# Kernel tuning notes

Measured on AMD Instinct MI355X. Metric: run time of the kernel, lower is better.

Reference implementation:

```python
import jax, jax.numpy as jnp
import numpy as np

B, N_LINES, C_FEAT = 16, 200, 64
H_IMG = W_IMG = 256
NUM_BINS = 32
LINE_LENGTH = 64
LINE_LENGTH_MINUS_1_HALF = (LINE_LENGTH - 1) / 2.0
MIN_CONTINUOUS_DISTANCE = 6.0
FUNCTION_AMPLITUDE = 0.43
FUNCTION_SLOPE = 0.5
EPS = 1e-05


def _unnorm(coord, size):
    # torch grid_sample align_corners=False: pixel = ((g + 1) * size - 1) / 2
    return ((coord + 1.0) * size - 1.0) * 0.5


def _gather2d(img, yi, xi, valid):
    # img (B,C,H,W); yi/xi (B,N,L) int32 in-range; zeros padding via valid mask
    g = jax.vmap(lambda im, yy, xx: im[:, yy, xx])(img, yi, xi)  # (B,C,N,L)
    return g * valid[:, None].astype(img.dtype)


def grid_sample_nearest(img, grid):
    _, _, H, W = img.shape
    x = _unnorm(grid[..., 0], W)
    y = _unnorm(grid[..., 1], H)
    xi = jnp.round(x).astype(jnp.int32)
    yi = jnp.round(y).astype(jnp.int32)
    valid = (xi >= 0) & (xi < W) & (yi >= 0) & (yi < H)
    return _gather2d(img, jnp.clip(yi, 0, H - 1), jnp.clip(xi, 0, W - 1), valid)


def grid_sample_bilinear(img, grid):
    _, _, H, W = img.shape
    x = _unnorm(grid[..., 0], W)
    y = _unnorm(grid[..., 1], H)
    x0 = jnp.floor(x)
    y0 = jnp.floor(y)
    wx1 = x - x0
    wy1 = y - y0
    x0i = x0.astype(jnp.int32)
    y0i = y0.astype(jnp.int32)
    out = jnp.zeros(img.shape[:2] + grid.shape[1:3], dtype=img.dtype)
    for dx, wx in ((0, 1.0 - wx1), (1, wx1)):
        for dy, wy in ((0, 1.0 - wy1), (1, wy1)):
            xi = x0i + dx
            yi = y0i + dy
            valid = (xi >= 0) & (xi < W) & (yi >= 0) & (yi < H)
            g = _gather2d(img, jnp.clip(yi, 0, H - 1), jnp.clip(xi, 0, W - 1), valid)
            out = out + g * (wx * wy)[:, None]
    return out


def setup_inputs() -> dict:
    key = jax.random.key(0)
    k = jax.random.split(key, 6)
    image = jax.random.uniform(k[0], (B, 3, H_IMG, W_IMG), dtype=jnp.float32)
    feature = jax.random.normal(k[1], (B, C_FEAT, H_IMG, W_IMG), dtype=jnp.float32)
    pose = jnp.concatenate([
        jnp.tile(jnp.eye(3, dtype=jnp.float32).reshape(1, 9), (B, 1)),
        jnp.tile(jnp.array([[0.0, 0.0, 0.5]], dtype=jnp.float32), (B, 1)),
    ], axis=-1)  # identity rotation, 0.5m in front of camera
    camera_data = jnp.tile(
        jnp.array([[float(W_IMG), float(H_IMG), 300.0, 300.0, 128.0, 128.0]], dtype=jnp.float32),
        (B, 1))  # [w, h, fx, fy, cx, cy]
    centers = jax.random.normal(k[2], (B, N_LINES, 3), dtype=jnp.float32) * 0.05
    normals = jax.random.normal(k[3], (B, N_LINES, 3), dtype=jnp.float32)
    normals = normals / jnp.linalg.norm(normals, axis=-1, keepdims=True)
    dists = jnp.full((B, N_LINES, 2), 0.02, dtype=jnp.float32)
    template_view = jnp.concatenate([centers, normals, dists], axis=-1)  # (B,N,8)
    fore_hist = jax.random.uniform(k[4], (B, NUM_BINS ** 3), dtype=jnp.float32)
    back_hist = jax.random.uniform(k[5], (B, NUM_BINS ** 3), dtype=jnp.float32)
    return {"image": image, "feature": feature,
            "init_body2view_pose_data": pose, "camera_data": camera_data,
            "template_view": template_view, "fore_hist": fore_hist,
            "back_hist": back_hist}


def reference(image, feature, init_body2view_pose_data, camera_data, template_view,
              fore_hist, back_hist):
    R = init_body2view_pose_data[:, :9].reshape(-1, 3, 3)
    t = init_body2view_pose_data[:, 9:]
    centers_in_body = template_view[..., :3]
    normals_in_body = template_view[..., 3:6]
    fg_dist = template_view[..., 6]
    bg_dist = template_view[..., 7]

    # transform / rotate (p3d @ R^T + t)
    centers_in_view = jnp.einsum('bnj,bij->bni', centers_in_body, R) + t[:, None]
    normals_in_view = jnp.einsum('bnj,bij->bni', normals_in_body, R)

    # project_p3d
    z = centers_in_view[..., 2]
    valid1 = z > 1e-4
    p2d = centers_in_view[..., :2] / jnp.maximum(z, 1e-4)[..., None]
    f = camera_data[:, 2:4]
    c = camera_data[:, 4:6]
    size = camera_data[:, :2]
    centers_in_image = p2d * f[:, None] + c[:, None]
    in_b = (centers_in_image >= 0) & (centers_in_image <= size[:, None] - 1)
    centers_valid = valid1 & in_b[..., 0] & in_b[..., 1]

    n2 = normals_in_view[..., :2]
    normals_in_image = n2 / jnp.maximum(jnp.linalg.norm(n2, axis=-1, keepdims=True), 1e-12)

    cur_fg = fg_dist * f[:, 0:1] / z
    cur_bg = bg_dist * f[:, 0:1] / z
    continuous_distance = jnp.minimum(cur_fg, cur_bg)  # fscale = 1 in forward
    valid_data_line = (continuous_distance >= MIN_CONTINUOUS_DISTANCE) & centers_valid

    width, height = feature.shape[2], feature.shape[3]

    # build search-line sample points: (B,N,L,2)
    step = jnp.arange(LINE_LENGTH, dtype=centers_in_image.dtype) - LINE_LENGTH_MINUS_1_HALF
    points = centers_in_image[:, :, None, :] + step[None, None, :, None] * normals_in_image[:, :, None, :]

    def _in_bounds(p):
        return (p[..., 0] >= 0) & (p[..., 0] < width) & (p[..., 1] >= 0) & (p[..., 1] < height)

    valid_data_line = valid_data_line & _in_bounds(points[:, :, 0]) & _in_bounds(points[:, :, -1])

    grid = jnp.stack([points[..., 0] / width * 2 - 1,
                      points[..., 1] / height * 2 - 1], axis=-1)

    # nearest sample of RGB image -> histogram fg/bg probability lookup
    lines_image = grid_sample_nearest(image, grid)  # (B,3,N,L)
    bins = jnp.clip((lines_image * NUM_BINS).astype(jnp.int32), 0, NUM_BINS - 1)
    hist_idx = (bins[:, 0] * NUM_BINS + bins[:, 1]) * NUM_BINS + bins[:, 2]  # (B,N,L)
    pf = jax.vmap(lambda h, i: h[i])(fore_hist, hist_idx)
    pb = jax.vmap(lambda h, i: h[i])(back_hist, hist_idx)
    zero_idx = (pf < EPS) & (pb < EPS)
    pf = jnp.where(zero_idx, EPS, pf)
    pb = jnp.where(zero_idx, EPS, pb)
    psum = pf + pb
    pf = pf / psum  # lines_image_pf_segments (second eps/normalize pass is a no-op)
    pb = pb / psum  # lines_image_pb_segments

    lines_feature = grid_sample_bilinear(feature, grid)  # (B,C,N,L)
    lines_amplitude = jnp.full(pf.shape[:2], FUNCTION_AMPLITUDE, dtype=feature.dtype)
    lines_slope = jnp.full(pf.shape[:2], FUNCTION_SLOPE, dtype=feature.dtype)

    return (normals_in_image, centers_in_image, centers_in_body, pf, pb,
            valid_data_line, lines_amplitude, lines_slope, lines_feature)
```

## Files before the change

### kernel.cpp

```cpp
#include <hip/hip_runtime.h>

#define BN     16
#define NLINES 200
#define CFEAT  64
#define HIMG   256
#define WIMG   256
#define LLEN   64
#define NBINS  32

#define O_NORM   0
#define O_CIMG   6400
#define O_CBODY  12800
#define O_PF     22400
#define O_PB     227200
#define O_VALID  432000
#define O_AMP    435200
#define O_SLOPE  438400
#define O_FEAT   441600

#define NPTS (BN*NLINES*LLEN)

struct LineGeom {
  float cix, ciy;
  float nix, niy;
  float cb0, cb1, cb2;
  bool  vdl;
};

__device__ __forceinline__ LineGeom compute_line(
    const float* __restrict__ pose, const float* __restrict__ cam,
    const float* __restrict__ tv, int b, int n)
{
  const float* P = pose + b*12;
  float R00=P[0],R01=P[1],R02=P[2];
  float R10=P[3],R11=P[4],R12=P[5];
  float R20=P[6],R21=P[7],R22=P[8];
  float t0=P[9], t1=P[10], t2=P[11];
  const float* C = cam + b*6;
  float sx=C[0], sy=C[1], fx=C[2], fy=C[3];
  float cx=C[4], cy=C[5];
  const float* T = tv + (b*NLINES + n)*8;
  float cb0=T[0], cb1=T[1], cb2=T[2];
  float nb0=T[3], nb1=T[4], nb2=T[5];
  float fg=T[6],  bg=T[7];

  float cv0 = R00*cb0 + R01*cb1 + R02*cb2 + t0;
  float cv1 = R10*cb0 + R11*cb1 + R12*cb2 + t1;
  float cv2 = R20*cb0 + R21*cb1 + R22*cb2 + t2;
  float nv0 = R00*nb0 + R01*nb1 + R02*nb2;
  float nv1 = R10*nb0 + R11*nb1 + R12*nb2;

  float z  = cv2;
  float zc = fmaxf(z, 1e-4f);
  float cix = (cv0/zc)*fx + cx;
  float ciy = (cv1/zc)*fy + cy;
  bool inb = (cix >= 0.f) && (cix <= sx - 1.f) && (ciy >= 0.f) && (ciy <= sy - 1.f);
  bool centers_valid = (z > 1e-4f) && inb;

  float nrm = fmaxf(sqrtf(nv0*nv0 + nv1*nv1), 1e-12f);
  float nix = nv0/nrm, niy = nv1/nrm;

  float contd = fminf(fg*fx/z, bg*fx/z);
  bool vdl = (contd >= 6.0f) && centers_valid;

  float px0 = cix + (-31.5f)*nix, py0 = ciy + (-31.5f)*niy;
  float px1 = cix + ( 31.5f)*nix, py1 = ciy + ( 31.5f)*niy;
  vdl = vdl && (px0 >= 0.f) && (px0 < 256.f) && (py0 >= 0.f) && (py0 < 256.f)
            && (px1 >= 0.f) && (px1 < 256.f) && (py1 >= 0.f) && (py1 < 256.f);

  LineGeom g;
  g.cix = cix; g.ciy = ciy; g.nix = nix; g.niy = niy;
  g.cb0 = cb0; g.cb1 = cb1; g.cb2 = cb2; g.vdl = vdl;
  return g;
}

__device__ __forceinline__ void point_xy(const LineGeom& g, int i, float& x, float& y)
{
  float s  = (float)i - 31.5f;
  float px = g.cix + s*g.nix;
  float py = g.ciy + s*g.niy;
  float gx = px/256.0f*2.0f - 1.0f;
  float gy = py/256.0f*2.0f - 1.0f;
  x = ((gx + 1.0f)*256.0f - 1.0f)*0.5f;
  y = ((gy + 1.0f)*256.0f - 1.0f)*0.5f;
}

template <bool PRE>
__device__ __forceinline__ void points_body(const float* __restrict__ image,
                                            const float* __restrict__ pose,
                                            const float* __restrict__ cam,
                                            const float* __restrict__ tv,
                                            const float* __restrict__ fore,
                                            const float* __restrict__ back,
                                            float* __restrict__ out,
                                            int4*  __restrict__ offs,
                                            float4* __restrict__ wts)
{
  int tid = blockIdx.x*256 + threadIdx.x;
  int i  = tid & 63;
  int ln = tid >> 6;
  int n  = ln % NLINES;
  int b  = ln / NLINES;

  LineGeom g = compute_line(pose, cam, tv, b, n);

  float x, y;
  point_xy(g, i, x, y);

  float xr = rintf(x), yr = rintf(y);
  int xi = (int)xr, yi = (int)yr;
  bool v = (xi >= 0) && (xi < WIMG) && (yi >= 0) && (yi < HIMG);
  int xc = min(max(xi, 0), WIMG-1), yc = min(max(yi, 0), HIMG-1);
  const float* ib = image + (size_t)b*3*HIMG*WIMG + yc*WIMG + xc;
  float r0 = v ? ib[0]           : 0.f;
  float r1 = v ? ib[HIMG*WIMG]   : 0.f;
  float r2 = v ? ib[2*HIMG*WIMG] : 0.f;

  int b0 = min(max((int)(r0*32.f), 0), NBINS-1);
  int b1 = min(max((int)(r1*32.f), 0), NBINS-1);
  int b2 = min(max((int)(r2*32.f), 0), NBINS-1);
  int hidx = (b0*NBINS + b1)*NBINS + b2;

  float pf = fore[b*NBINS*NBINS*NBINS + hidx];
  float pb = back[b*NBINS*NBINS*NBINS + hidx];
  if (pf < 1e-5f && pb < 1e-5f) { pf = 1e-5f; pb = 1e-5f; }
  float ps = pf + pb;
  pf /= ps; pb /= ps;

  out[O_PF + ln*LLEN + i] = pf;
  out[O_PB + ln*LLEN + i] = pb;

  if (i == 0) {
    out[O_NORM  + ln*2 + 0] = g.nix;
    out[O_NORM  + ln*2 + 1] = g.niy;
    out[O_CIMG  + ln*2 + 0] = g.cix;
    out[O_CIMG  + ln*2 + 1] = g.ciy;
    out[O_CBODY + ln*3 + 0] = g.cb0;
    out[O_CBODY + ln*3 + 1] = g.cb1;
    out[O_CBODY + ln*3 + 2] = g.cb2;
    out[O_VALID + ln] = g.vdl ? 1.0f : 0.0f;
    out[O_AMP   + ln] = 0.43f;
    out[O_SLOPE + ln] = 0.5f;
  }

  if (PRE) {
    float x0f = floorf(x), y0f = floorf(y);
    float wx1 = x - x0f, wy1 = y - y0f;
    float wx0 = 1.0f - wx1, wy0 = 1.0f - wy1;
    int x0 = (int)x0f, y0 = (int)y0f;
    int x1 = x0 + 1,  y1 = y0 + 1;
    bool vx0 = (x0 >= 0) && (x0 < WIMG);
    bool vx1 = (x1 >= 0) && (x1 < WIMG);
    bool vy0 = (y0 >= 0) && (y0 < HIMG);
    bool vy1 = (y1 >= 0) && (y1 < HIMG);
    float4 w;
    w.x = wx0*wy0 * ((vx0 && vy0) ? 1.f : 0.f);
    w.y = wx1*wy0 * ((vx1 && vy0) ? 1.f : 0.f);
    w.z = wx0*wy1 * ((vx0 && vy1) ? 1.f : 0.f);
    w.w = wx1*wy1 * ((vx1 && vy1) ? 1.f : 0.f);
    int xc0 = min(max(x0,0), WIMG-1), xc1 = min(max(x1,0), WIMG-1);
    int yc0 = min(max(y0,0), HIMG-1), yc1 = min(max(y1,0), HIMG-1);
    int4 o;
    o.x = yc0*WIMG + xc0;
    o.y = yc0*WIMG + xc1;
    o.z = yc1*WIMG + xc0;
    o.w = yc1*WIMG + xc1;
    offs[tid] = o;
    wts[tid]  = w;
  }
}

__global__ __launch_bounds__(256)
void contour_points_pre_kernel(const float* __restrict__ image,
                               const float* __restrict__ pose,
                               const float* __restrict__ cam,
                               const float* __restrict__ tv,
                               const float* __restrict__ fore,
                               const float* __restrict__ back,
                               float* __restrict__ out,
                               int4*  __restrict__ offs,
                               float4* __restrict__ wts)
{
  points_body<true>(image, pose, cam, tv, fore, back, out, offs, wts);
}

__global__ __launch_bounds__(256)
void contour_points_kernel(const float* __restrict__ image,
                           const float* __restrict__ pose,
                           const float* __restrict__ cam,
                           const float* __restrict__ tv,
                           const float* __restrict__ fore,
                           const float* __restrict__ back,
                           float* __restrict__ out)
{
  points_body<false>(image, pose, cam, tv, fore, back, out, nullptr, nullptr);
}

__global__ __launch_bounds__(256)
void contour_gather2_kernel(const float* __restrict__ feature,
                            const int4*  __restrict__ offs,
                            const float4* __restrict__ wts,
                            float* __restrict__ out)
{
  int bid = blockIdx.x;
  int xcd = bid & 7;
  int q   = bid >> 3;
  int j   = q % 50;
  int ug  = q / 50;
  int u   = ug*8 + xcd;
  int b   = u >> 5;
  int c2  = u & 31;
  int c   = c2 << 1;

  int idx = j*256 + (int)threadIdx.x;
  int n   = idx >> 6;
  int i   = idx & 63;

  int p = (b*NLINES + n)*LLEN + i;
  int4   o = offs[p];
  float4 w = wts[p];

  const float* f0 = feature + ((size_t)(b*CFEAT + c) << 16);
  const float* f1 = f0 + (1 << 16);

  float a00 = f0[o.x], a01 = f0[o.y], a02 = f0[o.z], a03 = f0[o.w];
  float a10 = f1[o.x], a11 = f1[o.y], a12 = f1[o.z], a13 = f1[o.w];
  float v0 = w.x*a00 + w.y*a01 + w.z*a02 + w.w*a03;
  float v1 = w.x*a10 + w.y*a11 + w.z*a12 + w.w*a13;

  size_t ob = (size_t)O_FEAT + (((size_t)(b*CFEAT + c))*NLINES + n)*LLEN + i;
  out[ob] = v0;
  out[ob + (size_t)(NLINES*LLEN)] = v1;
}

__global__ __launch_bounds__(256)
void contour_feature_kernel(const float* __restrict__ feature,
                            const float* __restrict__ pose,
                            const float* __restrict__ cam,
                            const float* __restrict__ tv,
                            float* __restrict__ out)
{
  int ln = blockIdx.x;
  int n  = ln % NLINES;
  int b  = ln / NLINES;
  int t  = threadIdx.x;
  int i  = t & 63;
  int w  = t >> 6;

  LineGeom g = compute_line(pose, cam, tv, b, n);
  float x, y;
  point_xy(g, i, x, y);

  float x0f = floorf(x), y0f = floorf(y);
  float wx1 = x - x0f, wy1 = y - y0f;
  float wx0 = 1.0f - wx1, wy0 = 1.0f - wy1;
  int x0 = (int)x0f, y0 = (int)y0f;
  int x1 = x0 + 1,  y1 = y0 + 1;
  bool vx0 = (x0 >= 0) && (x0 < WIMG);
  bool vx1 = (x1 >= 0) && (x1 < WIMG);
  bool vy0 = (y0 >= 0) && (y0 < HIMG);
  bool vy1 = (y1 >= 0) && (y1 < HIMG);
  float w00 = wx0*wy0 * ((vx0 && vy0) ? 1.f : 0.f);
  float w10 = wx1*wy0 * ((vx1 && vy0) ? 1.f : 0.f);
  float w01 = wx0*wy1 * ((vx0 && vy1) ? 1.f : 0.f);
  float w11 = wx1*wy1 * ((vx1 && vy1) ? 1.f : 0.f);
  int xc0 = min(max(x0,0), WIMG-1), xc1 = min(max(x1,0), WIMG-1);
  int yc0 = min(max(y0,0), HIMG-1), yc1 = min(max(y1,0), HIMG-1);
  int off00 = yc0*WIMG + xc0;
  int off10 = yc0*WIMG + xc1;
  int off01 = yc1*WIMG + xc0;
  int off11 = yc1*WIMG + xc1;

  const float* fbase = feature + (size_t)b*CFEAT*HIMG*WIMG;
  size_t obase = (size_t)O_FEAT + (((size_t)b*CFEAT)*NLINES + n)*LLEN + i;

  #pragma unroll
  for (int k = 0; k < 16; ++k) {
    int c = w*16 + k;
    const float* fc = fbase + (size_t)c*HIMG*WIMG;
    float val = w00*fc[off00] + w10*fc[off10]
              + w01*fc[off01] + w11*fc[off11];
    out[obase + (size_t)c*NLINES*LLEN] = val;
  }
}

extern "C" void kernel_launch(void* const* d_in, const int* in_sizes, int n_in,
                              void* d_out, int out_size, void* d_ws, size_t ws_size,
                              hipStream_t stream) {
  const float* image   = (const float*)d_in[0];
  const float* feature = (const float*)d_in[1];
  const float* pose    = (const float*)d_in[2];
  const float* cam     = (const float*)d_in[3];
  const float* tv      = (const float*)d_in[4];
  const float* fore    = (const float*)d_in[5];
  const float* back    = (const float*)d_in[6];
  float* out = (float*)d_out;

  const size_t need = (size_t)NPTS * (sizeof(int4) + sizeof(float4));
  if (ws_size >= need) {
    int4*   offs = (int4*)d_ws;
    float4* wts  = (float4*)((char*)d_ws + (size_t)NPTS*sizeof(int4));
    contour_points_pre_kernel<<<NPTS/256, 256, 0, stream>>>(
        image, pose, cam, tv, fore, back, out, offs, wts);
    contour_gather2_kernel<<<(BN*CFEAT*NLINES*LLEN)/(2*256), 256, 0, stream>>>(
        feature, offs, wts, out);
  } else {
    contour_points_kernel<<<NPTS/256, 256, 0, stream>>>(
        image, pose, cam, tv, fore, back, out);
    contour_feature_kernel<<<BN*NLINES, 256, 0, stream>>>(
        feature, pose, cam, tv, out);
  }
}
```

Baseline: 425.9 us.

## Recompute line geometry in gather kernel and fetch bilinear pairs as float2

Removes the precomputed offset/weight workspace and has the feature gather recompute each sample's line geometry and bilinear coordinates. Each thread now handles four channels instead of two, and it reads the two horizontally adjacent texels of each row with a single 8-byte load. The x index is clamped to a base column, and the weights are remapped so border cases stay correct. This saves the workspace write and read traffic and halves the number of scattered loads. The cost is redoing the geometry math once per four channels, and the 8-byte loads may be misaligned when the column index is odd.

Measured after the change: 414.4 us. 2.7% less time.

```diff
diff --git a/kernel.cpp b/kernel.cpp
--- a/kernel.cpp
+++ b/kernel.cpp
@@ -85,16 +85,14 @@
   y = ((gy + 1.0f)*256.0f - 1.0f)*0.5f;
 }
 
-template <bool PRE>
-__device__ __forceinline__ void points_body(const float* __restrict__ image,
-                                            const float* __restrict__ pose,
-                                            const float* __restrict__ cam,
-                                            const float* __restrict__ tv,
-                                            const float* __restrict__ fore,
-                                            const float* __restrict__ back,
-                                            float* __restrict__ out,
-                                            int4*  __restrict__ offs,
-                                            float4* __restrict__ wts)
+__global__ __launch_bounds__(256)
+void contour_points_kernel(const float* __restrict__ image,
+                           const float* __restrict__ pose,
+                           const float* __restrict__ cam,
+                           const float* __restrict__ tv,
+                           const float* __restrict__ fore,
+                           const float* __restrict__ back,
+                           float* __restrict__ out)
 {
   int tid = blockIdx.x*256 + threadIdx.x;
   int i  = tid & 63;
@@ -142,64 +140,13 @@
     out[O_AMP   + ln] = 0.43f;
     out[O_SLOPE + ln] = 0.5f;
   }
-
-  if (PRE) {
-    float x0f = floorf(x), y0f = floorf(y);
-    float wx1 = x - x0f, wy1 = y - y0f;
-    float wx0 = 1.0f - wx1, wy0 = 1.0f - wy1;
-    int x0 = (int)x0f, y0 = (int)y0f;
-    int x1 = x0 + 1,  y1 = y0 + 1;
-    bool vx0 = (x0 >= 0) && (x0 < WIMG);
-    bool vx1 = (x1 >= 0) && (x1 < WIMG);
-    bool vy0 = (y0 >= 0) && (y0 < HIMG);
-    bool vy1 = (y1 >= 0) && (y1 < HIMG);
-    float4 w;
-    w.x = wx0*wy0 * ((vx0 && vy0) ? 1.f : 0.f);
-    w.y = wx1*wy0 * ((vx1 && vy0) ? 1.f : 0.f);
-    w.z = wx0*wy1 * ((vx0 && vy1) ? 1.f : 0.f);
-    w.w = wx1*wy1 * ((vx1 && vy1) ? 1.f : 0.f);
-    int xc0 = min(max(x0,0), WIMG-1), xc1 = min(max(x1,0), WIMG-1);
-    int yc0 = min(max(y0,0), HIMG-1), yc1 = min(max(y1,0), HIMG-1);
-    int4 o;
-    o.x = yc0*WIMG + xc0;
-    o.y = yc0*WIMG + xc1;
-    o.z = yc1*WIMG + xc0;
-    o.w = yc1*WIMG + xc1;
-    offs[tid] = o;
-    wts[tid]  = w;
-  }
 }
 
 __global__ __launch_bounds__(256)
-void contour_points_pre_kernel(const float* __restrict__ image,
-                               const float* __restrict__ pose,
-                               const float* __restrict__ cam,
-                               const float* __restrict__ tv,
-                               const float* __restrict__ fore,
-                               const float* __restrict__ back,
-                               float* __restrict__ out,
-                               int4*  __restrict__ offs,
-                               float4* __restrict__ wts)
-{
-  points_body<true>(image, pose, cam, tv, fore, back, out, offs, wts);
-}
-
-__global__ __launch_bounds__(256)
-void contour_points_kernel(const float* __restrict__ image,
-                           const float* __restrict__ pose,
-                           const float* __restrict__ cam,
-                           const float* __restrict__ tv,
-                           const float* __restrict__ fore,
-                           const float* __restrict__ back,
-                           float* __restrict__ out)
-{
-  points_body<false>(image, pose, cam, tv, fore, back, out, nullptr, nullptr);
-}
-
-__global__ __launch_bounds__(256)
-void contour_gather2_kernel(const float* __restrict__ feature,
-                            const int4*  __restrict__ offs,
-                            const float4* __restrict__ wts,
+void contour_gather4_kernel(const float* __restrict__ feature,
+                            const float* __restrict__ pose,
+                            const float* __restrict__ cam,
+                            const float* __restrict__ tv,
                             float* __restrict__ out)
 {
   int bid = blockIdx.x;
@@ -208,44 +155,12 @@
   int j   = q % 50;
   int ug  = q / 50;
   int u   = ug*8 + xcd;
-  int b   = u >> 5;
-  int c2  = u & 31;
-  int c   = c2 << 1;
+  int b   = u >> 4;
+  int c   = (u & 15) << 2;
 
   int idx = j*256 + (int)threadIdx.x;
   int n   = idx >> 6;
   int i   = idx & 63;
-
-  int p = (b*NLINES + n)*LLEN + i;
-  int4   o = offs[p];
-  float4 w = wts[p];
-
-  const float* f0 = feature + ((size_t)(b*CFEAT + c) << 16);
-  const float* f1 = f0 + (1 << 16);
-
-  float a00 = f0[o.x], a01 = f0[o.y], a02 = f0[o.z], a03 = f0[o.w];
-  float a10 = f1[o.x], a11 = f1[o.y], a12 = f1[o.z], a13 = f1[o.w];
-  float v0 = w.x*a00 + w.y*a01 + w.z*a02 + w.w*a03;
-  float v1 = w.x*a10 + w.y*a11 + w.z*a12 + w.w*a13;
-
-  size_t ob = (size_t)O_FEAT + (((size_t)(b*CFEAT + c))*NLINES + n)*LLEN + i;
-  out[ob] = v0;
-  out[ob + (size_t)(NLINES*LLEN)] = v1;
-}
-
-__global__ __launch_bounds__(256)
-void contour_feature_kernel(const float* __restrict__ feature,
-                            const float* __restrict__ pose,
-                            const float* __restrict__ cam,
-                            const float* __restrict__ tv,
-                            float* __restrict__ out)
-{
-  int ln = blockIdx.x;
-  int n  = ln % NLINES;
-  int b  = ln / NLINES;
-  int t  = threadIdx.x;
-  int i  = t & 63;
-  int w  = t >> 6;
 
   LineGeom g = compute_line(pose, cam, tv, b, n);
   float x, y;
@@ -260,27 +175,37 @@
   bool vx1 = (x1 >= 0) && (x1 < WIMG);
   bool vy0 = (y0 >= 0) && (y0 < HIMG);
   bool vy1 = (y1 >= 0) && (y1 < HIMG);
-  float w00 = wx0*wy0 * ((vx0 && vy0) ? 1.f : 0.f);
-  float w10 = wx1*wy0 * ((vx1 && vy0) ? 1.f : 0.f);
-  float w01 = wx0*wy1 * ((vx0 && vy1) ? 1.f : 0.f);
-  float w11 = wx1*wy1 * ((vx1 && vy1) ? 1.f : 0.f);
-  int xc0 = min(max(x0,0), WIMG-1), xc1 = min(max(x1,0), WIMG-1);
-  int yc0 = min(max(y0,0), HIMG-1), yc1 = min(max(y1,0), HIMG-1);
-  int off00 = yc0*WIMG + xc0;
-  int off10 = yc0*WIMG + xc1;
-  int off01 = yc1*WIMG + xc0;
-  int off11 = yc1*WIMG + xc1;
-
-  const float* fbase = feature + (size_t)b*CFEAT*HIMG*WIMG;
-  size_t obase = (size_t)O_FEAT + (((size_t)b*CFEAT)*NLINES + n)*LLEN + i;
-
+
+  int xc0 = min(max(x0, 0), WIMG-1);
+  int xc1 = min(max(x1, 0), WIMG-1);
+  int xb  = min(max(x0, 0), WIMG-2);
+  int yb0 = min(max(y0, 0), HIMG-1);
+  int yb1 = min(max(y1, 0), HIMG-1);
+
+  float fx0 = vx0 ? wx0 : 0.f;
+  float fx1 = vx1 ? wx1 : 0.f;
+  float wa = ((xc0 == xb)   ? fx0 : 0.f) + ((xc1 == xb)   ? fx1 : 0.f);
+  float wb = ((xc0 == xb+1) ? fx0 : 0.f) + ((xc1 == xb+1) ? fx1 : 0.f);
+  float wyA = vy0 ? wy0 : 0.f;
+  float wyB = vy1 ? wy1 : 0.f;
+
+  const float* base = feature + ((size_t)(b*CFEAT + c) << 16);
+  int o0 = yb0*WIMG + xb;
+  int o1 = yb1*WIMG + xb;
+
+  float2 r0[4], r1[4];
   #pragma unroll
-  for (int k = 0; k < 16; ++k) {
-    int c = w*16 + k;
-    const float* fc = fbase + (size_t)c*HIMG*WIMG;
-    float val = w00*fc[off00] + w10*fc[off10]
-              + w01*fc[off01] + w11*fc[off11];
-    out[obase + (size_t)c*NLINES*LLEN] = val;
+  for (int k = 0; k < 4; ++k) {
+    __builtin_memcpy(&r0[k], base + (size_t)k*65536 + o0, 8);
+    __builtin_memcpy(&r1[k], base + (size_t)k*65536 + o1, 8);
+  }
+
+  size_t ob = (size_t)O_FEAT + (((size_t)(b*CFEAT + c))*NLINES + n)*LLEN + i;
+  #pragma unroll
+  for (int k = 0; k < 4; ++k) {
+    float v = wyA*(wa*r0[k].x + wb*r0[k].y)
+            + wyB*(wa*r1[k].x + wb*r1[k].y);
+    out[ob + (size_t)k*(NLINES*LLEN)] = v;
   }
 }
 
@@ -296,18 +221,8 @@
   const float* back    = (const float*)d_in[6];
   float* out = (float*)d_out;
 
-  const size_t need = (size_t)NPTS * (sizeof(int4) + sizeof(float4));
-  if (ws_size >= need) {
-    int4*   offs = (int4*)d_ws;
-    float4* wts  = (float4*)((char*)d_ws + (size_t)NPTS*sizeof(int4));
-    contour_points_pre_kernel<<<NPTS/256, 256, 0, stream>>>(
-        image, pose, cam, tv, fore, back, out, offs, wts);
-    contour_gather2_kernel<<<(BN*CFEAT*NLINES*LLEN)/(2*256), 256, 0, stream>>>(
-        feature, offs, wts, out);
-  } else {
-    contour_points_kernel<<<NPTS/256, 256, 0, stream>>>(
-        image, pose, cam, tv, fore, back, out);
-    contour_feature_kernel<<<BN*NLINES, 256, 0, stream>>>(
-        feature, pose, cam, tv, out);
-  }
-}
+  contour_points_kernel<<<NPTS/256, 256, 0, stream>>>(
+      image, pose, cam, tv, fore, back, out);
+  contour_gather4_kernel<<<(BN*CFEAT*NLINES*LLEN)/(4*256), 256, 0, stream>>>(
+      feature, pose, cam, tv, out);
+}
```
